# Optimization experiments

Measured on AMD Instinct MI355X. Metric: run time of the kernel, lower is better.

## Reference

```python
import jax, jax.numpy as jnp
import numpy as np

K = 8
NUM_BLOCKS = 12

def knn_idx(xyz, k):
    # xyz: (B,3,N). kNN in Euclidean space (self included), like gutil.group.
    sq = jnp.sum(xyz * xyz, axis=1)                      # (B,N)
    inner = jnp.einsum('bdn,bdm->bnm', xyz, xyz)         # (B,N,N)
    dist = sq[:, :, None] - 2.0 * inner + sq[:, None, :]
    _, idx = jax.lax.top_k(-dist, k)                     # (B,N,k)
    return idx

def gather_neighbors(points, idx):
    # points: (B,d,N), idx: (B,N,k) -> grouped (B,d,k,N)  [gutil.group_point]
    g = jax.vmap(lambda p, i: p[:, i])(points, idx)      # (B,d,N,k)
    return jnp.transpose(g, (0, 1, 3, 2))

def setup_inputs() -> dict:
    key = jax.random.key(0)
    ks = jax.random.split(key, 6)
    B, N, D = 4, 4096, 128
    return {
        'xyz': jax.random.normal(ks[0], (B, 3, N), dtype=jnp.float32),
        'points': jax.random.normal(ks[1], (B, D, N), dtype=jnp.float32),
        'conv_w1': jax.random.normal(ks[2], (NUM_BLOCKS, D, D), dtype=jnp.float32) * 0.05,
        'conv_w2': jax.random.normal(ks[3], (NUM_BLOCKS, D, D), dtype=jnp.float32) * 0.05,
        'w_center': jax.random.normal(ks[4], (6, D), dtype=jnp.float32) * 0.05,
        'w_neighbor': jax.random.normal(ks[5], (6, D), dtype=jnp.float32) * 0.05,
    }

def reference(xyz, points, conv_w1, conv_w2, w_center, w_neighbor):
    # kNN indices depend only on xyz -> computed once (idx==0 branch in torch).
    idx = knn_idx(xyz, K)
    inv = 1.0 / (K + 1)
    for i in range(NUM_BLOCKS):
        shortcut = points
        p = jax.nn.relu(points)                              # (B,d,N)
        grouped = gather_neighbors(p, idx)                   # (B,d,K,N)
        center = jnp.einsum('oi,bin->bon', conv_w1[i], p)    # 1x1 conv on center
        gnn_sum = jnp.einsum('oi,bikn->bon', conv_w2[i], grouped)  # conv + sum over K
        # mean over concat([center(1), grouped(K)]) along neighbor dim + residual
        points = (center + gnn_sum) * inv + shortcut
        if i == NUM_BLOCKS - 1:
            pxyz = jnp.einsum('oi,bin->bon', w_center, p)            # (B,6,N)
            gxyz_sum = jnp.einsum('oi,bikn->bon', w_neighbor, grouped)
            new_xyz = (pxyz + gxyz_sum) * inv                        # (B,6,N)
            B, _, N = xyz.shape
            new_xyz = new_xyz.reshape(B, 3, 2, N) + xyz[:, :, None, :]
            new_xyz = new_xyz.reshape(B, 3, 2 * N)
            return (new_xyz, points)
```

## Files before the change

### kernel.cpp

```cpp
#include <hip/hip_runtime.h>
#include <math.h>

#define BB 4
#define NN 4096
#define DD 128
#define KK 8
#define NBLK 12

typedef __attribute__((ext_vector_type(8))) short short8;
typedef __attribute__((ext_vector_type(4))) float f32x4;

__device__ inline ushort bf16_rn(float x) {
    uint u = __float_as_uint(x);
    u = (u + 0x7FFFu + ((u >> 16) & 1u)) >> 16;
    return (ushort)u;
}
__device__ inline float bf16_f(ushort h) { return __uint_as_float(((uint)h) << 16); }

__global__ __launch_bounds__(512) void knn_kernel(const float* __restrict__ xyz,
                                                  int* __restrict__ idx) {
    __shared__ float xs[NN], ys[NN], zs[NN], sq[NN];
    const int b = blockIdx.y;
    const float* xb = xyz + (size_t)b * 3 * NN;
    for (int i = threadIdx.x; i < NN; i += 512) {
        float x = xb[i], y = xb[NN + i], z = xb[2 * NN + i];
        xs[i] = x; ys[i] = y; zs[i] = z;
        sq[i] = __fadd_rn(__fadd_rn(__fmul_rn(x, x), __fmul_rn(y, y)),
                          __fmul_rn(z, z));
    }
    __syncthreads();

    const int wave = threadIdx.x >> 6;
    const int lane = threadIdx.x & 63;
    const int n = blockIdx.x * 8 + wave;
    const float qx = xs[n], qy = ys[n], qz = zs[n], qsq = sq[n];

    float d[KK];
    int id[KK];
#pragma unroll
    for (int j = 0; j < KK; ++j) { d[j] = INFINITY; id[j] = -1; }

    for (int j = 0; j < NN / 256; ++j) {
        const int m0 = j * 256 + lane * 4;
        const float4 vx = *(const float4*)&xs[m0];
        const float4 vy = *(const float4*)&ys[m0];
        const float4 vz = *(const float4*)&zs[m0];
        const float4 vq = *(const float4*)&sq[m0];
#pragma unroll
        for (int e = 0; e < 4; ++e) {
            const float cx = (&vx.x)[e], cy = (&vy.x)[e], cz = (&vz.x)[e];
            const float cq = (&vq.x)[e];
            float inner = __fadd_rn(__fadd_rn(__fmul_rn(qx, cx),
                                              __fmul_rn(qy, cy)),
                                    __fmul_rn(qz, cz));
            float dist = __fadd_rn(__fsub_rn(qsq, __fmul_rn(2.0f, inner)), cq);
            if (dist < d[KK - 1]) {
                d[KK - 1] = dist; id[KK - 1] = m0 + e;
#pragma unroll
                for (int t = KK - 1; t > 0; --t) {
                    if (d[t] < d[t - 1]) {
                        float td = d[t]; d[t] = d[t - 1]; d[t - 1] = td;
                        int ti = id[t]; id[t] = id[t - 1]; id[t - 1] = ti;
                    }
                }
            }
        }
    }

    int out[KK];
#pragma unroll
    for (int it = 0; it < KK; ++it) {
        float hd = d[0];
        int hi = id[0];
#pragma unroll
        for (int s = 32; s; s >>= 1) {
            float od = __shfl_xor(hd, s, 64);
            int oi = __shfl_xor(hi, s, 64);
            if (od < hd || (od == hd && oi < hi)) { hd = od; hi = oi; }
        }
        out[it] = hi;
        if (hd == d[0] && hi == id[0]) {
#pragma unroll
            for (int t = 0; t < KK - 1; ++t) { d[t] = d[t + 1]; id[t] = id[t + 1]; }
            d[KK - 1] = INFINITY; id[KK - 1] = -1;
        }
    }

    if (lane == 0) {
        int* op = idx + ((size_t)b * NN + n) * KK;
        *(int4*)op       = make_int4(out[0], out[1], out[2], out[3]);
        *(int4*)(op + 4) = make_int4(out[4], out[5], out[6], out[7]);
    }
}

__global__ __launch_bounds__(256) void prep_w(const float* __restrict__ w1,
                                              const float* __restrict__ w2,
                                              ushort* __restrict__ whi,
                                              ushort* __restrict__ wlo) {
    const int e = blockIdx.x * 256 + threadIdx.x;
    const int l = e >> 15;
    const int rem = e & 32767;
    const int r = rem >> 8;
    const int k = rem & 255;
    float w = (k < 128) ? w1[((size_t)l * 128 + r) * 128 + k]
                        : w2[((size_t)l * 128 + r) * 128 + (k - 128)];
    ushort h = bf16_rn(w);
    whi[e] = h;
    wlo[e] = bf16_rn(w - bf16_f(h));
}

__global__ __launch_bounds__(256) void transpose_pts(const float* __restrict__ pts,
                                                     float* __restrict__ ptsT) {
    __shared__ float t[32][33];
    const int b = blockIdx.z;
    const int c0 = blockIdx.y * 32;
    const int n0 = blockIdx.x * 32;
    const int tx = threadIdx.x & 31;
    const int ty = threadIdx.x >> 5;
#pragma unroll
    for (int q = 0; q < 4; ++q)
        t[ty + 8 * q][tx] = pts[((size_t)b * DD + c0 + ty + 8 * q) * NN + n0 + tx];
    __syncthreads();
#pragma unroll
    for (int q = 0; q < 4; ++q)
        ptsT[((size_t)b * NN + n0 + ty + 8 * q) * DD + c0 + tx] = t[tx][ty + 8 * q];
}

__global__ __launch_bounds__(256) void fused_block(const float* __restrict__ ptsT_in,
                                                   const int* __restrict__ idx,
                                                   const ushort* __restrict__ whi,
                                                   const ushort* __restrict__ wlo,
                                                   float* __restrict__ ptsT_out,
                                                   float* __restrict__ out_std,
                                                   const float* __restrict__ wc,
                                                   const float* __restrict__ wn,
                                                   const float* __restrict__ xyz,
                                                   float* __restrict__ out_xyz,
                                                   const int last) {
    __shared__ __align__(16) char xt[32768];
    __shared__ float sc[32][132];
    char* xt_hi = xt;
    char* xt_lo = xt + 16384;

    const int bid = blockIdx.x;
    const int xcd = bid & 7;
    const int b = xcd >> 1;
    const int colbase = (((xcd & 1) << 6) + (bid >> 3)) * 32;

    const int w = threadIdx.x >> 6;
    const int lane = threadIdx.x & 63;

    const float* baseT = ptsT_in + (size_t)b * NN * DD;

    {
        const int row0 = w * 8;
        const int iv = idx[((size_t)b * NN + colbase + row0) * KK + lane];

        for (int i = 0; i < 8; ++i) {
            const int n_loc = row0 + i;
            const int n = colbase + n_loc;
            int nb[KK];
#pragma unroll
            for (int j = 0; j < KK; ++j) nb[j] = __shfl(iv, i * 8 + j, 64);

            const float2 c2 = *(const float2*)(baseT + (size_t)n * DD + 2 * lane);
            float gx = 0.0f, gy = 0.0f;
#pragma unroll
            for (int j = 0; j < KK; ++j) {
                const float2 u = *(const float2*)(baseT + (size_t)nb[j] * DD + 2 * lane);
                gx += fmaxf(u.x, 0.0f);
                gy += fmaxf(u.y, 0.0f);
            }
            const float px = fmaxf(c2.x, 0.0f);
            const float py = fmaxf(c2.y, 0.0f);

            sc[n_loc][2 * lane]     = c2.x;
            sc[n_loc][2 * lane + 1] = c2.y;

            ushort phx = bf16_rn(px), phy = bf16_rn(py);
            ushort plx = bf16_rn(px - bf16_f(phx)), ply = bf16_rn(py - bf16_f(phy));
            ushort ghx = bf16_rn(gx), ghy = bf16_rn(gy);
            ushort glx = bf16_rn(gx - bf16_f(ghx)), gly = bf16_rn(gy - bf16_f(ghy));

            const int kP = 2 * lane;
            const int kG = 128 + 2 * lane;
            const int byP = n_loc * 512 + ((((kP >> 3) ^ (n_loc & 7))) << 4) + ((kP & 7) << 1);
            const int byG = n_loc * 512 + ((((kG >> 3) ^ (n_loc & 7))) << 4) + ((kG & 7) << 1);
            *(uint*)(xt_hi + byP) = (uint)phx | ((uint)phy << 16);
            *(uint*)(xt_lo + byP) = (uint)plx | ((uint)ply << 16);
            *(uint*)(xt_hi + byG) = (uint)ghx | ((uint)ghy << 16);
            *(uint*)(xt_lo + byG) = (uint)glx | ((uint)gly << 16);

            if (last) {
                float s0, s1, s2, s3, s4, s5;
                {
                    const int c0 = 2 * lane, c1 = 2 * lane + 1;
                    s0 = px * wc[0 * 128 + c0] + py * wc[0 * 128 + c1]
                       + gx * wn[0 * 128 + c0] + gy * wn[0 * 128 + c1];
                    s1 = px * wc[1 * 128 + c0] + py * wc[1 * 128 + c1]
                       + gx * wn[1 * 128 + c0] + gy * wn[1 * 128 + c1];
                    s2 = px * wc[2 * 128 + c0] + py * wc[2 * 128 + c1]
                       + gx * wn[2 * 128 + c0] + gy * wn[2 * 128 + c1];
                    s3 = px * wc[3 * 128 + c0] + py * wc[3 * 128 + c1]
                       + gx * wn[3 * 128 + c0] + gy * wn[3 * 128 + c1];
                    s4 = px * wc[4 * 128 + c0] + py * wc[4 * 128 + c1]
                       + gx * wn[4 * 128 + c0] + gy * wn[4 * 128 + c1];
                    s5 = px * wc[5 * 128 + c0] + py * wc[5 * 128 + c1]
                       + gx * wn[5 * 128 + c0] + gy * wn[5 * 128 + c1];
                }
#pragma unroll
                for (int st = 32; st; st >>= 1) {
                    s0 += __shfl_xor(s0, st, 64);
                    s1 += __shfl_xor(s1, st, 64);
                    s2 += __shfl_xor(s2, st, 64);
                    s3 += __shfl_xor(s3, st, 64);
                    s4 += __shfl_xor(s4, st, 64);
                    s5 += __shfl_xor(s5, st, 64);
                }
                if (lane < 6) {
                    float v = s0;
                    v = (lane == 1) ? s1 : v;
                    v = (lane == 2) ? s2 : v;
                    v = (lane == 3) ? s3 : v;
                    v = (lane == 4) ? s4 : v;
                    v = (lane == 5) ? s5 : v;
                    const int dd = lane >> 1, h = lane & 1;
                    const float xv = xyz[((size_t)b * 3 + dd) * NN + n];
                    out_xyz[(((size_t)b * 3 + dd) * 2 + h) * NN + n] =
                        v * (1.0f / 9.0f) + xv;
                }
            }
        }
    }
    __syncthreads();

    const int ln15 = lane & 15;
    const int kl = lane >> 4;

    f32x4 acc[2][2] = {};
#pragma unroll
    for (int pass = 0; pass < 3; ++pass) {
        const ushort* Wp = (pass == 2) ? wlo : whi;
        const char* Xp = (pass == 1) ? xt_lo : xt_hi;
#pragma unroll
        for (int ks = 0; ks < 8; ++ks) {
            short8 a[2];
#pragma unroll
            for (int rt = 0; rt < 2; ++rt) {
                const int row = w * 32 + rt * 16 + ln15;
                a[rt] = *(const short8*)(Wp + (size_t)row * 256 + ks * 32 + kl * 8);
            }
            short8 bf[2];
#pragma unroll
            for (int nt = 0; nt < 2; ++nt) {
                const int n_loc = nt * 16 + ln15;
                const int by = n_loc * 512 + (((ks * 4 + kl) ^ (n_loc & 7)) << 4);
                bf[nt] = *(const short8*)(Xp + by);
            }
#pragma unroll
            for (int rt = 0; rt < 2; ++rt)
#pragma unroll
                for (int nt = 0; nt < 2; ++nt)
                    acc[rt][nt] = __builtin_amdgcn_mfma_f32_16x16x32_bf16(
                        a[rt], bf[nt], acc[rt][nt], 0, 0, 0);
        }
    }

    const float inv = 1.0f / 9.0f;
#pragma unroll
    for (int rt = 0; rt < 2; ++rt) {
#pragma unroll
        for (int nt = 0; nt < 2; ++nt) {
            const int row = w * 32 + rt * 16 + (lane >> 4) * 4;
            const int nl = nt * 16 + ln15;
            const int n = colbase + nl;
            const float4 scv = *(const float4*)&sc[nl][row];
            float v0 = acc[rt][nt][0] * inv + scv.x;
            float v1 = acc[rt][nt][1] * inv + scv.y;
            float v2 = acc[rt][nt][2] * inv + scv.z;
            float v3 = acc[rt][nt][3] * inv + scv.w;
            if (!last) {
                *(float4*)(ptsT_out + ((size_t)b * NN + n) * DD + row) =
                    make_float4(v0, v1, v2, v3);
            } else {
                out_std[((size_t)b * DD + row + 0) * NN + n] = v0;
                out_std[((size_t)b * DD + row + 1) * NN + n] = v1;
                out_std[((size_t)b * DD + row + 2) * NN + n] = v2;
                out_std[((size_t)b * DD + row + 3) * NN + n] = v3;
            }
        }
    }
}

extern "C" void kernel_launch(void* const* d_in, const int* in_sizes, int n_in,
                              void* d_out, int out_size, void* d_ws, size_t ws_size,
                              hipStream_t stream) {
    const float* xyz    = (const float*)d_in[0];
    const float* points = (const float*)d_in[1];
    const float* w1     = (const float*)d_in[2];
    const float* w2     = (const float*)d_in[3];
    const float* wc     = (const float*)d_in[4];
    const float* wn     = (const float*)d_in[5];
    float* out = (float*)d_out;

    const size_t feat = (size_t)BB * DD * NN;
    char* ws = (char*)d_ws;
    int*    idx  = (int*)ws;
    ushort* whi  = (ushort*)(ws + 524288);
    ushort* wlo  = (ushort*)(ws + 524288 + 786432);
    float*  pT0  = (float*)(ws + 524288 + 2 * 786432);
    float*  pT1  = pT0 + feat;

    knn_kernel<<<dim3(NN / 8, BB), 512, 0, stream>>>(xyz, idx);
    prep_w<<<dim3(12 * 128 * 256 / 256), 256, 0, stream>>>(w1, w2, whi, wlo);
    transpose_pts<<<dim3(NN / 32, DD / 32, BB), 256, 0, stream>>>(points, pT0);

    float* out_pts = out + (size_t)BB * 3 * 2 * NN;
    float* bufs[2] = {pT0, pT1};
    for (int i = 0; i < NBLK; ++i) {
        const int last = (i == NBLK - 1);
        fused_block<<<dim3(512), 256, 0, stream>>>(
            bufs[i & 1], idx, whi + (size_t)i * 32768, wlo + (size_t)i * 32768,
            bufs[(i + 1) & 1], out_pts, wc, wn, xyz, out, last);
    }
}
```

Measured before the change: 338.7 us.

## Prune kNN insertions with a wave-wide threshold and prefetch neighbor gathers

The kNN kernel now keeps a wave-wide threshold, the minimum over lanes of each lane's current worst candidate. It skips the sorted-insert path when no lane has a candidate that beats both its local worst and that threshold, which cuts divergent insertion work. The threshold is refreshed after every 256-point chunk, at the cost of a short shuffle reduction. Separately, the block kernel's gather loop software-pipelines the center and neighbor loads for row i+1 while row i is being processed, hiding global memory latency at the cost of extra registers.

```diff
diff --git a/kernel.cpp b/kernel.cpp
--- a/kernel.cpp
+++ b/kernel.cpp
@@ -40,6 +40,8 @@
 #pragma unroll
     for (int j = 0; j < KK; ++j) { d[j] = INFINITY; id[j] = -1; }
 
+    float thr = INFINITY;
+
     for (int j = 0; j < NN / 256; ++j) {
         const int m0 = j * 256 + lane * 4;
         const float4 vx = *(const float4*)&xs[m0];
@@ -54,17 +56,24 @@
                                               __fmul_rn(qy, cy)),
                                     __fmul_rn(qz, cz));
             float dist = __fadd_rn(__fsub_rn(qsq, __fmul_rn(2.0f, inner)), cq);
-            if (dist < d[KK - 1]) {
-                d[KK - 1] = dist; id[KK - 1] = m0 + e;
-#pragma unroll
-                for (int t = KK - 1; t > 0; --t) {
-                    if (d[t] < d[t - 1]) {
-                        float td = d[t]; d[t] = d[t - 1]; d[t - 1] = td;
-                        int ti = id[t]; id[t] = id[t - 1]; id[t - 1] = ti;
+            const bool ins = (dist < d[KK - 1]) && (dist <= thr);
+            if (__any(ins)) {
+                if (ins) {
+                    d[KK - 1] = dist; id[KK - 1] = m0 + e;
+#pragma unroll
+                    for (int t = KK - 1; t > 0; --t) {
+                        if (d[t] < d[t - 1]) {
+                            float td = d[t]; d[t] = d[t - 1]; d[t - 1] = td;
+                            int ti = id[t]; id[t] = id[t - 1]; id[t - 1] = ti;
+                        }
                     }
                 }
             }
         }
+        float t = d[KK - 1];
+#pragma unroll
+        for (int s = 32; s; s >>= 1) t = fminf(t, __shfl_xor(t, s, 64));
+        thr = t;
     }
 
     int out[KK];
@@ -156,20 +165,37 @@
         const int row0 = w * 8;
         const int iv = idx[((size_t)b * NN + colbase + row0) * KK + lane];
 
+        float2 c2, u[KK];
+        {
+            int nb[KK];
+#pragma unroll
+            for (int j = 0; j < KK; ++j) nb[j] = __shfl(iv, j, 64);
+            c2 = *(const float2*)(baseT + (size_t)(colbase + row0) * DD + 2 * lane);
+#pragma unroll
+            for (int j = 0; j < KK; ++j)
+                u[j] = *(const float2*)(baseT + (size_t)nb[j] * DD + 2 * lane);
+        }
+
+#pragma unroll
         for (int i = 0; i < 8; ++i) {
+            float2 c2n, un[KK];
+            if (i < 7) {
+                int nbn[KK];
+#pragma unroll
+                for (int j = 0; j < KK; ++j) nbn[j] = __shfl(iv, (i + 1) * 8 + j, 64);
+                c2n = *(const float2*)(baseT + (size_t)(colbase + row0 + i + 1) * DD + 2 * lane);
+#pragma unroll
+                for (int j = 0; j < KK; ++j)
+                    un[j] = *(const float2*)(baseT + (size_t)nbn[j] * DD + 2 * lane);
+            }
+
             const int n_loc = row0 + i;
             const int n = colbase + n_loc;
-            int nb[KK];
-#pragma unroll
-            for (int j = 0; j < KK; ++j) nb[j] = __shfl(iv, i * 8 + j, 64);
-
-            const float2 c2 = *(const float2*)(baseT + (size_t)n * DD + 2 * lane);
             float gx = 0.0f, gy = 0.0f;
 #pragma unroll
             for (int j = 0; j < KK; ++j) {
-                const float2 u = *(const float2*)(baseT + (size_t)nb[j] * DD + 2 * lane);
-                gx += fmaxf(u.x, 0.0f);
-                gy += fmaxf(u.y, 0.0f);
+                gx += fmaxf(u[j].x, 0.0f);
+                gy += fmaxf(u[j].y, 0.0f);
             }
             const float px = fmaxf(c2.x, 0.0f);
             const float py = fmaxf(c2.y, 0.0f);
@@ -230,6 +256,12 @@
                         v * (1.0f / 9.0f) + xv;
                 }
             }
+
+            if (i < 7) {
+                c2 = c2n;
+#pragma unroll
+                for (int j = 0; j < KK; ++j) u[j] = un[j];
+            }
         }
     }
     __syncthreads();
```

Measured after the change: 332.3 us. Within noise of the previous version (-1.9%).

## Double fused block threads, vectorize gather to float4, and split MFMA tiles per wave

Applied to the files above, without the earlier changes.

The fused block kernel now launches 512 threads instead of 256. Each wave gathers 4 points, with half-waves handling one point each, using float4 neighbor loads issued all up front. The GEMM phase gives each wave a 16-row tile instead of 32 rows and interleaves the hi/lo split-bf16 MFMAs within one k-loop. The aim is more memory-level parallelism for the gather and more waves to hide latency. The cost is higher register pressure from the 8 buffered float4 loads, and the launch bound of 512 threads with 4 blocks may limit registers per thread.

```diff
diff --git a/kernel.cpp b/kernel.cpp
--- a/kernel.cpp
+++ b/kernel.cpp
@@ -126,17 +126,17 @@
         ptsT[((size_t)b * NN + n0 + ty + 8 * q) * DD + c0 + tx] = t[tx][ty + 8 * q];
 }
 
-__global__ __launch_bounds__(256) void fused_block(const float* __restrict__ ptsT_in,
-                                                   const int* __restrict__ idx,
-                                                   const ushort* __restrict__ whi,
-                                                   const ushort* __restrict__ wlo,
-                                                   float* __restrict__ ptsT_out,
-                                                   float* __restrict__ out_std,
-                                                   const float* __restrict__ wc,
-                                                   const float* __restrict__ wn,
-                                                   const float* __restrict__ xyz,
-                                                   float* __restrict__ out_xyz,
-                                                   const int last) {
+__global__ __launch_bounds__(512, 4) void fused_block(const float* __restrict__ ptsT_in,
+                                                      const int* __restrict__ idx,
+                                                      const ushort* __restrict__ whi,
+                                                      const ushort* __restrict__ wlo,
+                                                      float* __restrict__ ptsT_out,
+                                                      float* __restrict__ out_std,
+                                                      const float* __restrict__ wc,
+                                                      const float* __restrict__ wn,
+                                                      const float* __restrict__ xyz,
+                                                      float* __restrict__ out_xyz,
+                                                      const int last) {
     __shared__ __align__(16) char xt[32768];
     __shared__ float sc[32][132];
     char* xt_hi = xt;
@@ -149,145 +149,156 @@
 
     const int w = threadIdx.x >> 6;
     const int lane = threadIdx.x & 63;
+    const int half = lane >> 5;
+    const int l32 = lane & 31;
+    const int choff = 4 * l32;
+    const int row0 = w * 4;
 
     const float* baseT = ptsT_in + (size_t)b * NN * DD;
 
-    {
-        const int row0 = w * 8;
-        const int iv = idx[((size_t)b * NN + colbase + row0) * KK + lane];
-
-        for (int i = 0; i < 8; ++i) {
-            const int n_loc = row0 + i;
-            const int n = colbase + n_loc;
-            int nb[KK];
-#pragma unroll
-            for (int j = 0; j < KK; ++j) nb[j] = __shfl(iv, i * 8 + j, 64);
-
-            const float2 c2 = *(const float2*)(baseT + (size_t)n * DD + 2 * lane);
-            float gx = 0.0f, gy = 0.0f;
-#pragma unroll
-            for (int j = 0; j < KK; ++j) {
-                const float2 u = *(const float2*)(baseT + (size_t)nb[j] * DD + 2 * lane);
-                gx += fmaxf(u.x, 0.0f);
-                gy += fmaxf(u.y, 0.0f);
-            }
-            const float px = fmaxf(c2.x, 0.0f);
-            const float py = fmaxf(c2.y, 0.0f);
-
-            sc[n_loc][2 * lane]     = c2.x;
-            sc[n_loc][2 * lane + 1] = c2.y;
-
-            ushort phx = bf16_rn(px), phy = bf16_rn(py);
-            ushort plx = bf16_rn(px - bf16_f(phx)), ply = bf16_rn(py - bf16_f(phy));
-            ushort ghx = bf16_rn(gx), ghy = bf16_rn(gy);
-            ushort glx = bf16_rn(gx - bf16_f(ghx)), gly = bf16_rn(gy - bf16_f(ghy));
-
-            const int kP = 2 * lane;
-            const int kG = 128 + 2 * lane;
-            const int byP = n_loc * 512 + ((((kP >> 3) ^ (n_loc & 7))) << 4) + ((kP & 7) << 1);
-            const int byG = n_loc * 512 + ((((kG >> 3) ^ (n_loc & 7))) << 4) + ((kG & 7) << 1);
-            *(uint*)(xt_hi + byP) = (uint)phx | ((uint)phy << 16);
-            *(uint*)(xt_lo + byP) = (uint)plx | ((uint)ply << 16);
-            *(uint*)(xt_hi + byG) = (uint)ghx | ((uint)ghy << 16);
-            *(uint*)(xt_lo + byG) = (uint)glx | ((uint)gly << 16);
-
-            if (last) {
-                float s0, s1, s2, s3, s4, s5;
-                {
-                    const int c0 = 2 * lane, c1 = 2 * lane + 1;
-                    s0 = px * wc[0 * 128 + c0] + py * wc[0 * 128 + c1]
-                       + gx * wn[0 * 128 + c0] + gy * wn[0 * 128 + c1];
-                    s1 = px * wc[1 * 128 + c0] + py * wc[1 * 128 + c1]
-                       + gx * wn[1 * 128 + c0] + gy * wn[1 * 128 + c1];
-                    s2 = px * wc[2 * 128 + c0] + py * wc[2 * 128 + c1]
-                       + gx * wn[2 * 128 + c0] + gy * wn[2 * 128 + c1];
-                    s3 = px * wc[3 * 128 + c0] + py * wc[3 * 128 + c1]
-                       + gx * wn[3 * 128 + c0] + gy * wn[3 * 128 + c1];
-                    s4 = px * wc[4 * 128 + c0] + py * wc[4 * 128 + c1]
-                       + gx * wn[4 * 128 + c0] + gy * wn[4 * 128 + c1];
-                    s5 = px * wc[5 * 128 + c0] + py * wc[5 * 128 + c1]
-                       + gx * wn[5 * 128 + c0] + gy * wn[5 * 128 + c1];
-                }
-#pragma unroll
-                for (int st = 32; st; st >>= 1) {
-                    s0 += __shfl_xor(s0, st, 64);
-                    s1 += __shfl_xor(s1, st, 64);
-                    s2 += __shfl_xor(s2, st, 64);
-                    s3 += __shfl_xor(s3, st, 64);
-                    s4 += __shfl_xor(s4, st, 64);
-                    s5 += __shfl_xor(s5, st, 64);
-                }
-                if (lane < 6) {
-                    float v = s0;
-                    v = (lane == 1) ? s1 : v;
-                    v = (lane == 2) ? s2 : v;
-                    v = (lane == 3) ? s3 : v;
-                    v = (lane == 4) ? s4 : v;
-                    v = (lane == 5) ? s5 : v;
-                    const int dd = lane >> 1, h = lane & 1;
-                    const float xv = xyz[((size_t)b * 3 + dd) * NN + n];
-                    out_xyz[(((size_t)b * 3 + dd) * 2 + h) * NN + n] =
-                        v * (1.0f / 9.0f) + xv;
-                }
-            }
-        }
-    }
-    __syncthreads();
+    const int iv = idx[((size_t)b * NN + colbase + row0) * KK + (lane & 31)];
 
     const int ln15 = lane & 15;
     const int kl = lane >> 4;
 
-    f32x4 acc[2][2] = {};
-#pragma unroll
-    for (int pass = 0; pass < 3; ++pass) {
-        const ushort* Wp = (pass == 2) ? wlo : whi;
-        const char* Xp = (pass == 1) ? xt_lo : xt_hi;
-#pragma unroll
-        for (int ks = 0; ks < 8; ++ks) {
-            short8 a[2];
-#pragma unroll
-            for (int rt = 0; rt < 2; ++rt) {
-                const int row = w * 32 + rt * 16 + ln15;
-                a[rt] = *(const short8*)(Wp + (size_t)row * 256 + ks * 32 + kl * 8);
+#pragma unroll
+    for (int i = 0; i < 2; ++i) {
+        const int n_loc = row0 + 2 * i + half;
+        const int n = colbase + n_loc;
+
+        int nb[KK];
+#pragma unroll
+        for (int j = 0; j < KK; ++j) nb[j] = __shfl(iv, (2 * i + half) * 8 + j, 64);
+
+        const float4 c4 = *(const float4*)(baseT + (size_t)n * DD + choff);
+        float4 u[KK];
+#pragma unroll
+        for (int j = 0; j < KK; ++j)
+            u[j] = *(const float4*)(baseT + (size_t)nb[j] * DD + choff);
+
+        float g0 = 0.f, g1 = 0.f, g2 = 0.f, g3 = 0.f;
+#pragma unroll
+        for (int j = 0; j < KK; ++j) {
+            g0 += fmaxf(u[j].x, 0.f);
+            g1 += fmaxf(u[j].y, 0.f);
+            g2 += fmaxf(u[j].z, 0.f);
+            g3 += fmaxf(u[j].w, 0.f);
+        }
+        const float p0 = fmaxf(c4.x, 0.f);
+        const float p1 = fmaxf(c4.y, 0.f);
+        const float p2 = fmaxf(c4.z, 0.f);
+        const float p3 = fmaxf(c4.w, 0.f);
+
+        *(float4*)&sc[n_loc][choff] = c4;
+
+        ushort ph0 = bf16_rn(p0), ph1 = bf16_rn(p1), ph2 = bf16_rn(p2), ph3 = bf16_rn(p3);
+        ushort pl0 = bf16_rn(p0 - bf16_f(ph0)), pl1 = bf16_rn(p1 - bf16_f(ph1));
+        ushort pl2 = bf16_rn(p2 - bf16_f(ph2)), pl3 = bf16_rn(p3 - bf16_f(ph3));
+        ushort gh0 = bf16_rn(g0), gh1 = bf16_rn(g1), gh2 = bf16_rn(g2), gh3 = bf16_rn(g3);
+        ushort gl0 = bf16_rn(g0 - bf16_f(gh0)), gl1 = bf16_rn(g1 - bf16_f(gh1));
+        ushort gl2 = bf16_rn(g2 - bf16_f(gh2)), gl3 = bf16_rn(g3 - bf16_f(gh3));
+
+        const int gP = l32 >> 1;
+        const int sub = (l32 & 1) << 3;
+        const int byP = n_loc * 512 + ((gP ^ (n_loc & 7)) << 4) + sub;
+        const int byG = n_loc * 512 + (((16 + gP) ^ (n_loc & 7)) << 4) + sub;
+
+        *(unsigned long long*)(xt_hi + byP) =
+            (unsigned long long)ph0 | ((unsigned long long)ph1 << 16) |
+            ((unsigned long long)ph2 << 32) | ((unsigned long long)ph3 << 48);
+        *(unsigned long long*)(xt_lo + byP) =
+            (unsigned long long)pl0 | ((unsigned long long)pl1 << 16) |
+            ((unsigned long long)pl2 << 32) | ((unsigned long long)pl3 << 48);
+        *(unsigned long long*)(xt_hi + byG) =
+            (unsigned long long)gh0 | ((unsigned long long)gh1 << 16) |
+            ((unsigned long long)gh2 << 32) | ((unsigned long long)gh3 << 48);
+        *(unsigned long long*)(xt_lo + byG) =
+            (unsigned long long)gl0 | ((unsigned long long)gl1 << 16) |
+            ((unsigned long long)gl2 << 32) | ((unsigned long long)gl3 << 48);
+
+        if (last) {
+            float s0, s1, s2, s3, s4, s5;
+            {
+                const int c0 = choff, c1 = choff + 1, c2 = choff + 2, c3 = choff + 3;
+                s0 = p0 * wc[0 * 128 + c0] + p1 * wc[0 * 128 + c1] + p2 * wc[0 * 128 + c2] + p3 * wc[0 * 128 + c3]
+                   + g0 * wn[0 * 128 + c0] + g1 * wn[0 * 128 + c1] + g2 * wn[0 * 128 + c2] + g3 * wn[0 * 128 + c3];
+                s1 = p0 * wc[1 * 128 + c0] + p1 * wc[1 * 128 + c1] + p2 * wc[1 * 128 + c2] + p3 * wc[1 * 128 + c3]
+                   + g0 * wn[1 * 128 + c0] + g1 * wn[1 * 128 + c1] + g2 * wn[1 * 128 + c2] + g3 * wn[1 * 128 + c3];
+                s2 = p0 * wc[2 * 128 + c0] + p1 * wc[2 * 128 + c1] + p2 * wc[2 * 128 + c2] + p3 * wc[2 * 128 + c3]
+                   + g0 * wn[2 * 128 + c0] + g1 * wn[2 * 128 + c1] + g2 * wn[2 * 128 + c2] + g3 * wn[2 * 128 + c3];
+                s3 = p0 * wc[3 * 128 + c0] + p1 * wc[3 * 128 + c1] + p2 * wc[3 * 128 + c2] + p3 * wc[3 * 128 + c3]
+                   + g0 * wn[3 * 128 + c0] + g1 * wn[3 * 128 + c1] + g2 * wn[3 * 128 + c2] + g3 * wn[3 * 128 + c3];
+                s4 = p0 * wc[4 * 128 + c0] + p1 * wc[4 * 128 + c1] + p2 * wc[4 * 128 + c2] + p3 * wc[4 * 128 + c3]
+                   + g0 * wn[4 * 128 + c0] + g1 * wn[4 * 128 + c1] + g2 * wn[4 * 128 + c2] + g3 * wn[4 * 128 + c3];
+                s5 = p0 * wc[5 * 128 + c0] + p1 * wc[5 * 128 + c1] + p2 * wc[5 * 128 + c2] + p3 * wc[5 * 128 + c3]
+                   + g0 * wn[5 * 128 + c0] + g1 * wn[5 * 128 + c1] + g2 * wn[5 * 128 + c2] + g3 * wn[5 * 128 + c3];
             }
-            short8 bf[2];
-#pragma unroll
-            for (int nt = 0; nt < 2; ++nt) {
-                const int n_loc = nt * 16 + ln15;
-                const int by = n_loc * 512 + (((ks * 4 + kl) ^ (n_loc & 7)) << 4);
-                bf[nt] = *(const short8*)(Xp + by);
+#pragma unroll
+            for (int st = 16; st; st >>= 1) {
+                s0 += __shfl_xor(s0, st, 64);
+                s1 += __shfl_xor(s1, st, 64);
+                s2 += __shfl_xor(s2, st, 64);
+                s3 += __shfl_xor(s3, st, 64);
+                s4 += __shfl_xor(s4, st, 64);
+                s5 += __shfl_xor(s5, st, 64);
             }
-#pragma unroll
-            for (int rt = 0; rt < 2; ++rt)
-#pragma unroll
-                for (int nt = 0; nt < 2; ++nt)
-                    acc[rt][nt] = __builtin_amdgcn_mfma_f32_16x16x32_bf16(
-                        a[rt], bf[nt], acc[rt][nt], 0, 0, 0);
+            if (l32 < 6) {
+                float v = s0;
+                v = (l32 == 1) ? s1 : v;
+                v = (l32 == 2) ? s2 : v;
+                v = (l32 == 3) ? s3 : v;
+                v = (l32 == 4) ? s4 : v;
+                v = (l32 == 5) ? s5 : v;
+                const int dd = l32 >> 1, h = l32 & 1;
+                const float xv = xyz[((size_t)b * 3 + dd) * NN + n];
+                out_xyz[(((size_t)b * 3 + dd) * 2 + h) * NN + n] =
+                    v * (1.0f / 9.0f) + xv;
+            }
+        }
+    }
+    __syncthreads();
+
+    const int wrow = w * 16 + ln15;
+    f32x4 acc[2] = {};
+#pragma unroll
+    for (int ks = 0; ks < 8; ++ks) {
+        const short8 a_hi = *(const short8*)(whi + (size_t)wrow * 256 + ks * 32 + kl * 8);
+        const short8 a_lo = *(const short8*)(wlo + (size_t)wrow * 256 + ks * 32 + kl * 8);
+        short8 bfh[2], bfl[2];
+#pragma unroll
+        for (int nt = 0; nt < 2; ++nt) {
+            const int n_loc = nt * 16 + ln15;
+            const int by = n_loc * 512 + (((ks * 4 + kl) ^ (n_loc & 7)) << 4);
+            bfh[nt] = *(const short8*)(xt_hi + by);
+            bfl[nt] = *(const short8*)(xt_lo + by);
+        }
+#pragma unroll
+        for (int nt = 0; nt < 2; ++nt) {
+            acc[nt] = __builtin_amdgcn_mfma_f32_16x16x32_bf16(a_hi, bfh[nt], acc[nt], 0, 0, 0);
+            acc[nt] = __builtin_amdgcn_mfma_f32_16x16x32_bf16(a_hi, bfl[nt], acc[nt], 0, 0, 0);
+            acc[nt] = __builtin_amdgcn_mfma_f32_16x16x32_bf16(a_lo, bfh[nt], acc[nt], 0, 0, 0);
         }
     }
 
     const float inv = 1.0f / 9.0f;
-#pragma unroll
-    for (int rt = 0; rt < 2; ++rt) {
-#pragma unroll
-        for (int nt = 0; nt < 2; ++nt) {
-            const int row = w * 32 + rt * 16 + (lane >> 4) * 4;
-            const int nl = nt * 16 + ln15;
-            const int n = colbase + nl;
-            const float4 scv = *(const float4*)&sc[nl][row];
-            float v0 = acc[rt][nt][0] * inv + scv.x;
-            float v1 = acc[rt][nt][1] * inv + scv.y;
-            float v2 = acc[rt][nt][2] * inv + scv.z;
-            float v3 = acc[rt][nt][3] * inv + scv.w;
-            if (!last) {
-                *(float4*)(ptsT_out + ((size_t)b * NN + n) * DD + row) =
-                    make_float4(v0, v1, v2, v3);
-            } else {
-                out_std[((size_t)b * DD + row + 0) * NN + n] = v0;
-                out_std[((size_t)b * DD + row + 1) * NN + n] = v1;
-                out_std[((size_t)b * DD + row + 2) * NN + n] = v2;
-                out_std[((size_t)b * DD + row + 3) * NN + n] = v3;
-            }
+    const int orow = w * 16 + kl * 4;
+#pragma unroll
+    for (int nt = 0; nt < 2; ++nt) {
+        const int nl = nt * 16 + ln15;
+        const int n = colbase + nl;
+        const float4 scv = *(const float4*)&sc[nl][orow];
+        float v0 = acc[nt][0] * inv + scv.x;
+        float v1 = acc[nt][1] * inv + scv.y;
+        float v2 = acc[nt][2] * inv + scv.z;
+        float v3 = acc[nt][3] * inv + scv.w;
+        if (!last) {
+            *(float4*)(ptsT_out + ((size_t)b * NN + n) * DD + orow) =
+                make_float4(v0, v1, v2, v3);
+        } else {
+            out_std[((size_t)b * DD + orow + 0) * NN + n] = v0;
+            out_std[((size_t)b * DD + orow + 1) * NN + n] = v1;
+            out_std[((size_t)b * DD + orow + 2) * NN + n] = v2;
+            out_std[((size_t)b * DD + orow + 3) * NN + n] = v3;
         }
     }
 }
@@ -319,7 +330,7 @@
     float* bufs[2] = {pT0, pT1};
     for (int i = 0; i < NBLK; ++i) {
         const int last = (i == NBLK - 1);
-        fused_block<<<dim3(512), 256, 0, stream>>>(
+        fused_block<<<dim3(512), 512, 0, stream>>>(
             bufs[i & 1], idx, whi + (size_t)i * 32768, wlo + (size_t)i * 32768,
             bufs[(i + 1) & 1], out_pts, wc, wn, xyz, out, last);
     }
```

After: 296.3 us. -12.5%, faster.
